# Kernel optimization log

Hardware: AMD Instinct MI355X
Metric: run time of the kernel (lower is better)

## Reference

```python
import jax, jax.numpy as jnp
import numpy as np

INV_COEFF = 25.0
VAR_COEFF = 25.0
COV_COEFF = 1.0


def _cdist(a, b):
    # Euclidean pairwise distance, (B,N,C)x(B,M,C)->(B,N,M)
    a2 = jnp.sum(a * a, axis=-1)[:, :, None]
    b2 = jnp.sum(b * b, axis=-1)[:, None, :]
    d2 = a2 + b2 - 2.0 * jnp.einsum('bnc,bmc->bnm', a, b)
    return jnp.sqrt(jnp.maximum(d2, 0.0))


def _nn_match(input_maps, candidate_maps, distances, num_matches):
    # top-1 NN per input row, then keep the num_matches rows with the
    # smallest NN-distance, preserving original row order (matches the
    # torch sort/sort/mask + masked_select logic exactly).
    min_vals = jnp.min(distances, axis=-1)       # (B, N)
    nn_idx = jnp.argmin(distances, axis=-1)      # (B, N)
    order = jnp.argsort(min_vals, axis=1)[:, :num_matches]   # rows with smallest min-dist
    indices_selected = jnp.sort(order, axis=1)               # restore original order (B, M)
    nn_selected = jnp.take_along_axis(nn_idx, indices_selected, axis=1)  # (B, M)
    filt_in = jnp.take_along_axis(input_maps, indices_selected[..., None], axis=1)
    filt_cand = jnp.take_along_axis(candidate_maps, nn_selected[..., None], axis=1)
    return filt_in, filt_cand


def _vicreg_loss(x, y):
    # x, y: (B, M, C)
    B = x.shape[0]
    C = x.shape[-1]
    repr_loss = INV_COEFF * jnp.mean((x - y) ** 2)
    # gather_center: subtract batch mean (single-device equivalent)
    xc = x - jnp.mean(x, axis=0, keepdims=True)
    yc = y - jnp.mean(y, axis=0, keepdims=True)
    std_x = jnp.sqrt(jnp.var(xc, axis=0, ddof=1) + 1e-4)
    std_y = jnp.sqrt(jnp.var(yc, axis=0, ddof=1) + 1e-4)
    std_loss = VAR_COEFF * (jnp.mean(jax.nn.relu(1.0 - std_x)) / 2
                            + jnp.mean(jax.nn.relu(1.0 - std_y)) / 2)
    # covariance per location: permute to (M, B, C), center over batch
    xp = jnp.transpose(xc, (1, 0, 2))
    yp = jnp.transpose(yc, (1, 0, 2))
    xp = xp - jnp.mean(xp, axis=-2, keepdims=True)
    yp = yp - jnp.mean(yp, axis=-2, keepdims=True)
    cov_x = jnp.einsum('mnc,mnd->mcd', xp, xp) / (B - 1)
    cov_y = jnp.einsum('mnc,mnd->mcd', yp, yp) / (B - 1)
    off = 1.0 - jnp.eye(C, dtype=x.dtype)
    cov_loss = (jnp.sum((cov_x * off) ** 2, axis=(-2, -1)) / C / 2
                + jnp.sum((cov_y * off) ** 2, axis=(-2, -1)) / C / 2)
    cov_loss = COV_COEFF * jnp.mean(cov_loss)
    return repr_loss, std_loss, cov_loss


def _local_loss(maps_1, maps_2, location_1, location_2, num_matches):
    # L2-feature-space NN matching, both directions
    m1f_l2, m1nn_l2 = _nn_match(maps_1, maps_2, _cdist(maps_1, maps_2), num_matches)
    m2f_l2, m2nn_l2 = _nn_match(maps_2, maps_1, _cdist(maps_2, maps_1), num_matches)
    # location-space NN matching, both directions
    loc1 = location_1.reshape(location_1.shape[0], -1, location_1.shape[-1])
    loc2 = location_2.reshape(location_2.shape[0], -1, location_2.shape[-1])
    m1f_loc, m1nn_loc = _nn_match(maps_1, maps_2, _cdist(loc1, loc2), num_matches)
    m2f_loc, m2nn_loc = _nn_match(maps_2, maps_1, _cdist(loc2, loc1), num_matches)
    inv = var = cov = 0.0
    for a, b in ((m1f_l2, m1nn_l2), (m2f_l2, m2nn_l2),
                 (m1f_loc, m1nn_loc), (m2f_loc, m2nn_loc)):
        i, v, c = _vicreg_loss(a, b)
        inv = inv + i
        var = var + v
        cov = cov + c
    return inv + var + cov


def setup_inputs() -> dict:
    key = jax.random.key(0)
    k1, k2, k3, k4 = jax.random.split(key, 4)
    B, HW, C, H = 64, 784, 512, 28
    return {
        'maps_1': jax.random.normal(k1, (B, HW, C), dtype=jnp.float32),
        'maps_2': jax.random.normal(k2, (B, HW, C), dtype=jnp.float32),
        'location_1': jax.random.uniform(k3, (B, H, H, 2), dtype=jnp.float32),
        'location_2': jax.random.uniform(k4, (B, H, H, 2), dtype=jnp.float32),
        'num_matches': 256,
    }


def reference(maps_1, maps_2, location_1, location_2, num_matches):
    return _local_loss(maps_1, maps_2, location_1, location_2, num_matches)
```

## Files before the change

### kernel.cpp

```cpp
#include <hip/hip_runtime.h>
#include <stdint.h>

#define B 64
#define N 784
#define C 512
#define M 256

typedef unsigned long long u64;
typedef unsigned short u16;
typedef __attribute__((ext_vector_type(8))) short short8;
typedef __attribute__((ext_vector_type(4))) float f32x4;

static __device__ __forceinline__ u64 umin64(u64 a, u64 b) { return a < b ? a : b; }

static __device__ __forceinline__ u16 f2bf(float x) {
    unsigned u = __float_as_uint(x);
    return (u16)((u + 0x7FFFu + ((u >> 16) & 1u)) >> 16);
}
static __device__ __forceinline__ float b2f(u16 v) {
    return __uint_as_float((unsigned)v << 16);
}

static __device__ __forceinline__ void gload_lds16(const u16* g, u16* l) {
    __builtin_amdgcn_global_load_lds((const __attribute__((address_space(1))) void*)g,
                                     (__attribute__((address_space(3))) void*)l, 16, 0, 0);
}

__global__ __launch_bounds__(256) void convnorm_kernel(
    const float* __restrict__ m1, const float* __restrict__ m2,
    u16* __restrict__ abf, u16* __restrict__ bbf, float* __restrict__ nrm) {
    int w = blockIdx.x * 4 + (threadIdx.x >> 6);
    int lane = threadIdx.x & 63;
    if (w >= 2 * B * N) return;
    const float* src = (w < B * N) ? m1 : m2;
    u16* dst = (w < B * N) ? abf : bbf;
    int row = (w < B * N) ? w : w - B * N;
    const float4* p = (const float4*)(src + (size_t)row * C);
    u64* q = (u64*)(dst + (size_t)row * C);
    float s = 0.f;
#pragma unroll
    for (int i = 0; i < 2; ++i) {
        int idx = lane + i * 64;
        float4 v = p[idx];
        s += v.x * v.x + v.y * v.y + v.z * v.z + v.w * v.w;
        q[idx] = (u64)f2bf(v.x) | ((u64)f2bf(v.y) << 16) |
                 ((u64)f2bf(v.z) << 32) | ((u64)f2bf(v.w) << 48);
    }
#pragma unroll
    for (int off = 32; off > 0; off >>= 1) s += __shfl_down(s, off, 64);
    if (lane == 0) nrm[w] = s;
}

__global__ __launch_bounds__(256, 2) void feat_mfma_kernel(
    const u16* __restrict__ abf, const u16* __restrict__ bbf,
    const float* __restrict__ nrm, u64* __restrict__ rowkey) {
    int id = blockIdx.x;
    int xcd = id & 7;
    int q = id >> 3;
    int hi = q / 49, t49 = q - hi * 49;
    int b = hi * 8 + xcd;
    int tn = t49 / 7, tm = t49 - tn * 7;

    const int t = threadIdx.x;
    const int lane = t & 63, wv = t >> 6;
    const int wr = wv >> 1, wc = wv & 1;

    __shared__ __align__(16) u16 SM[2][2][128 * 64];
    __shared__ float sNa[128], sNb[128];

    const int row0 = tn * 128, col0 = tm * 128;
    if (t < 128) {
        int n = row0 + t;
        sNa[t] = (n < N) ? nrm[b * N + n] : __builtin_inff();
    } else {
        int m = col0 + (t - 128);
        sNb[t - 128] = (m < N) ? nrm[B * N + b * N + m] : __builtin_inff();
    }

    size_t aofs[4], bofs[4];
    int ldso[4];
#pragma unroll
    for (int s = 0; s < 4; ++s) {
        int c = (wv * 4 + s) * 64 + lane;
        int rl = c >> 3;
        int grp = (c & 7) ^ (rl & 7);
        int ga = row0 + rl; if (ga > N - 1) ga = N - 1;
        int gb = col0 + rl; if (gb > N - 1) gb = N - 1;
        aofs[s] = ((size_t)b * N + ga) * C + grp * 8;
        bofs[s] = ((size_t)b * N + gb) * C + grp * 8;
        ldso[s] = (wv * 4 + s) * 512;
    }

    f32x4 acc[4][4];
#pragma unroll
    for (int i = 0; i < 4; ++i)
#pragma unroll
        for (int j = 0; j < 4; ++j) acc[i][j] = (f32x4){0.f, 0.f, 0.f, 0.f};

#pragma unroll
    for (int s = 0; s < 4; ++s) {
        gload_lds16(abf + aofs[s], &SM[0][0][ldso[s]]);
        gload_lds16(bbf + bofs[s], &SM[0][1][ldso[s]]);
    }
    __syncthreads();

    for (int kt = 0; kt < 8; ++kt) {
        const int cur = kt & 1;
        if (kt < 7) {
            int ke = (kt + 1) * 64;
#pragma unroll
            for (int s = 0; s < 4; ++s) {
                gload_lds16(abf + aofs[s] + ke, &SM[cur ^ 1][0][ldso[s]]);
                gload_lds16(bbf + bofs[s] + ke, &SM[cur ^ 1][1][ldso[s]]);
            }
        }
        const u16* Als = SM[cur][0];
        const u16* Bls = SM[cur][1];
#pragma unroll
        for (int ks = 0; ks < 2; ++ks) {
            short8 afr[4], bfr[4];
            int cb = ks * 4 + (lane >> 4);
#pragma unroll
            for (int f = 0; f < 4; ++f) {
                int ra = wr * 64 + f * 16 + (lane & 15);
                afr[f] = *(const short8*)&Als[ra * 64 + ((cb ^ (ra & 7)) << 3)];
                int rb = wc * 64 + f * 16 + (lane & 15);
                bfr[f] = *(const short8*)&Bls[rb * 64 + ((cb ^ (rb & 7)) << 3)];
            }
#pragma unroll
            for (int fi = 0; fi < 4; ++fi)
#pragma unroll
                for (int fj = 0; fj < 4; ++fj)
                    acc[fi][fj] = __builtin_amdgcn_mfma_f32_16x16x32_bf16(
                        afr[fi], bfr[fj], acc[fi][fj], 0, 0, 0);
        }
        __syncthreads();
    }

    const int g4 = (lane >> 4) << 2;
    float na4[4][4], nb4[4];
#pragma unroll
    for (int fi = 0; fi < 4; ++fi) {
        float4 v = *(const float4*)&sNa[wr * 64 + fi * 16 + g4];
        na4[fi][0] = v.x; na4[fi][1] = v.y; na4[fi][2] = v.z; na4[fi][3] = v.w;
    }
#pragma unroll
    for (int fj = 0; fj < 4; ++fj) nb4[fj] = sNb[wc * 64 + fj * 16 + (lane & 15)];

    u64(*red)[33] = (u64(*)[33])SM;
    u64 ck[4] = {~0ull, ~0ull, ~0ull, ~0ull};
#pragma unroll
    for (int fi = 0; fi < 4; ++fi) {
        int rl = wr * 64 + fi * 16 + g4;
        u64 rk[4] = {~0ull, ~0ull, ~0ull, ~0ull};
#pragma unroll
        for (int fj = 0; fj < 4; ++fj) {
            unsigned colidx = (unsigned)(col0 + wc * 64 + fj * 16 + (lane & 15));
#pragma unroll
            for (int reg = 0; reg < 4; ++reg) {
                float d2 = fmaxf(na4[fi][reg] + nb4[fj] - 2.f * acc[fi][fj][reg], 0.f);
                u64 hv = ((u64)__float_as_uint(d2) << 32);
                rk[reg] = umin64(rk[reg], hv | colidx);
                ck[fj] = umin64(ck[fj], hv | (unsigned)(row0 + rl + reg));
            }
        }
#pragma unroll
        for (int reg = 0; reg < 4; ++reg)
            red[rl + reg][(wc << 4) | (lane & 15)] = rk[reg];
    }
#pragma unroll
    for (int fj = 0; fj < 4; ++fj) {
        u64 best = ck[fj];
        best = umin64(best, __shfl_xor(best, 16, 64));
        best = umin64(best, __shfl_xor(best, 32, 64));
        if (lane < 16) {
            int m = col0 + wc * 64 + fj * 16 + lane;
            if (m < N) atomicMin(&rowkey[(size_t)B * N + (size_t)b * N + m], best);
        }
    }
    __syncthreads();
    if (t < 128) {
        u64 best = red[t][0];
#pragma unroll
        for (int x = 1; x < 32; ++x) best = umin64(best, red[t][x]);
        int n = row0 + t;
        if (n < N) atomicMin(&rowkey[(size_t)b * N + n], best);
    }
}

__global__ __launch_bounds__(256) void loc_dist_kernel(
    const float* __restrict__ l1, const float* __restrict__ l2,
    u64* __restrict__ rowkey) {
    const int dir = blockIdx.z;
    const int b = blockIdx.y;
    const int t = threadIdx.x;
    const int n = blockIdx.x * 256 + t;
    __shared__ float2 s[N];
    const float* Ap = dir ? l2 : l1;
    const float* Bp = dir ? l1 : l2;
    for (int i = t; i < N; i += 256) s[i] = ((const float2*)Bp)[b * N + i];
    __syncthreads();
    if (n >= N) return;
    float2 a = ((const float2*)Ap)[b * N + n];
    float a2 = a.x * a.x + a.y * a.y;
    u64 best = ~0ull;
    for (int mm = 0; mm < N; ++mm) {
        float2 bb = s[mm];
        float d2 = a2 + (bb.x * bb.x + bb.y * bb.y) - 2.f * (a.x * bb.x + a.y * bb.y);
        unsigned vb = __float_as_uint(fmaxf(d2, 0.f));
        u64 kv = ((u64)vb << 32) | (unsigned)mm;
        best = kv < best ? kv : best;
    }
    rowkey[(size_t)(2 + dir) * B * N + (size_t)b * N + n] = best;
}

__global__ __launch_bounds__(256) void select_kernel(
    const u64* __restrict__ rowkey, int* __restrict__ sel_idx,
    int* __restrict__ nn_idx) {
    const int b = blockIdx.x;
    const int dir = blockIdx.y;
    const int t = threadIdx.x;
    __shared__ u64 sk[1024];
    const u64* rk = rowkey + (size_t)dir * B * N + (size_t)b * N;
    for (int i = t; i < 1024; i += 256)
        sk[i] = (i < N) ? ((rk[i] & 0xFFFFFFFF00000000ull) | (unsigned)i) : ~0ull;
    __syncthreads();
    for (unsigned k = 2; k <= 1024; k <<= 1) {
        for (unsigned j = k >> 1; j > 0; j >>= 1) {
            for (unsigned i = t; i < 1024; i += 256) {
                unsigned ixj = i ^ j;
                if (ixj > i) {
                    u64 x = sk[i], y = sk[ixj];
                    bool up = ((i & k) == 0);
                    if ((x > y) == up) { sk[i] = y; sk[ixj] = x; }
                }
            }
            __syncthreads();
        }
    }
    unsigned myidx = (unsigned)(sk[t] & 0xFFFFFFFFull);
    __syncthreads();
    unsigned* si = (unsigned*)sk;
    si[t] = myidx;
    __syncthreads();
    for (unsigned k = 2; k <= 256; k <<= 1) {
        for (unsigned j = k >> 1; j > 0; j >>= 1) {
            unsigned i = t, ixj = i ^ j;
            if (ixj > i) {
                unsigned x = si[i], y = si[ixj];
                bool up = ((i & k) == 0);
                if ((x > y) == up) { si[i] = y; si[ixj] = x; }
            }
            __syncthreads();
        }
    }
    int sel = (int)si[t];
    sel_idx[((size_t)dir * B + b) * M + t] = sel;
    nn_idx[((size_t)dir * B + b) * M + t] = (int)(unsigned)(rk[sel] & 0xFFFFFFFFull);
}

__global__ __launch_bounds__(256) void vicreg_mfma_kernel(
    const u16* __restrict__ abf, const u16* __restrict__ bbf,
    const int* __restrict__ sel_idx, const int* __restrict__ nn_idx,
    float* __restrict__ acc) {
    const int mloc = blockIdx.x;
    const int p = blockIdx.y;
    const int t = threadIdx.x;
    const int l = t & 63, w = t >> 6;

    __shared__ u16 Xs[64 * 128];
    __shared__ u16 Ys[64 * 128];
    __shared__ float colpart[4][128];
    __shared__ float Rsx[64], Rsy[64];
    __shared__ int xi[64], yi[64];
    __shared__ float redsc[4][4];

    if (t < 64) xi[t] = sel_idx[((size_t)p * B + t) * M + mloc];
    else if (t < 128) yi[t - 64] = nn_idx[((size_t)p * B + (t - 64)) * M + mloc];
    if (t < 128) { colpart[0][t] = 0.f; colpart[1][t] = 0.f;
                   colpart[2][t] = 0.f; colpart[3][t] = 0.f; }
    __syncthreads();

    const u16* Xg = (p & 1) ? bbf : abf;
    const u16* Yg = (p & 1) ? abf : bbf;
    unsigned xofs[4], yofs[4];
#pragma unroll
    for (int s = 0; s < 4; ++s) {
        int r = w * 16 + s * 4 + (l >> 4);
        int cs = (l & 15) ^ (r & 15);
        xofs[s] = (unsigned)((r * N + xi[r]) * C + cs * 8);
        yofs[s] = (unsigned)((r * N + yi[r]) * C + cs * 8);
    }

    f32x4 Gx[4], Gy[4], Z;
#pragma unroll
    for (int j = 0; j < 4; ++j) { Gx[j] = (f32x4){0,0,0,0}; Gy[j] = (f32x4){0,0,0,0}; }
    Z = (f32x4){0, 0, 0, 0};
    float stdacc = 0.f, covdacc = 0.f, reprp = 0.f;

    for (int kc = 0; kc < 4; ++kc) {
#pragma unroll
        for (int s = 0; s < 4; ++s) {
            gload_lds16(Xg + xofs[s] + kc * 128, &Xs[(w * 16 + s * 4) * 128]);
            gload_lds16(Yg + yofs[s] + kc * 128, &Ys[(w * 16 + s * 4) * 128]);
        }
        __syncthreads();

#pragma unroll
        for (int ks = 0; ks < 4; ++ks) {
            int cb = ks * 4 + (l >> 4);
            int pe = (cb ^ (l & 15)) << 3;
            short8 ax = *(const short8*)&Xs[((w << 4) + (l & 15)) * 128 + pe];
            short8 ay = *(const short8*)&Ys[((w << 4) + (l & 15)) * 128 + pe];
            short8 bx[4], by[4];
#pragma unroll
            for (int j = 0; j < 4; ++j) {
                bx[j] = *(const short8*)&Xs[(j * 16 + (l & 15)) * 128 + pe];
                by[j] = *(const short8*)&Ys[(j * 16 + (l & 15)) * 128 + pe];
            }
#pragma unroll
            for (int j = 0; j < 4; ++j) {
                Gx[j] = __builtin_amdgcn_mfma_f32_16x16x32_bf16(ax, bx[j], Gx[j], 0, 0, 0);
                Gy[j] = __builtin_amdgcn_mfma_f32_16x16x32_bf16(ay, by[j], Gy[j], 0, 0, 0);
            }
            Z = __builtin_amdgcn_mfma_f32_16x16x32_bf16(ax, ay, Z, 0, 0, 0);
        }

        {
            int cg = l & 31;
            int g2 = (w << 1) + (l >> 5);
            int c4 = cg << 2;
            int cc = c4 >> 3, h = (c4 >> 2) & 1;
            float s1x0 = 0, s1x1 = 0, s1x2 = 0, s1x3 = 0;
            float s2x0 = 0, s2x1 = 0, s2x2 = 0, s2x3 = 0;
            float s1y0 = 0, s1y1 = 0, s1y2 = 0, s1y3 = 0;
            float s2y0 = 0, s2y1 = 0, s2y2 = 0, s2y3 = 0;
#pragma unroll
            for (int rr = 0; rr < 8; ++rr) {
                int r = g2 * 8 + rr;
                int off = r * 128 + ((cc ^ (r & 15)) << 3) + h * 4;
                ushort4 vx = *(const ushort4*)&Xs[off];
                ushort4 vy = *(const ushort4*)&Ys[off];
                float x0 = b2f(vx.x), x1 = b2f(vx.y), x2 = b2f(vx.z), x3 = b2f(vx.w);
                float y0 = b2f(vy.x), y1 = b2f(vy.y), y2 = b2f(vy.z), y3 = b2f(vy.w);
                s1x0 += x0; s1x1 += x1; s1x2 += x2; s1x3 += x3;
                s2x0 = fmaf(x0, x0, s2x0); s2x1 = fmaf(x1, x1, s2x1);
                s2x2 = fmaf(x2, x2, s2x2); s2x3 = fmaf(x3, x3, s2x3);
                s1y0 += y0; s1y1 += y1; s1y2 += y2; s1y3 += y3;
                s2y0 = fmaf(y0, y0, s2y0); s2y1 = fmaf(y1, y1, s2y1);
                s2y2 = fmaf(y2, y2, s2y2); s2y3 = fmaf(y3, y3, s2y3);
            }
            s1x0 += __shfl_xor(s1x0, 32, 64); s1x1 += __shfl_xor(s1x1, 32, 64);
            s1x2 += __shfl_xor(s1x2, 32, 64); s1x3 += __shfl_xor(s1x3, 32, 64);
            s2x0 += __shfl_xor(s2x0, 32, 64); s2x1 += __shfl_xor(s2x1, 32, 64);
            s2x2 += __shfl_xor(s2x2, 32, 64); s2x3 += __shfl_xor(s2x3, 32, 64);
            s1y0 += __shfl_xor(s1y0, 32, 64); s1y1 += __shfl_xor(s1y1, 32, 64);
            s1y2 += __shfl_xor(s1y2, 32, 64); s1y3 += __shfl_xor(s1y3, 32, 64);
            s2y0 += __shfl_xor(s2y0, 32, 64); s2y1 += __shfl_xor(s2y1, 32, 64);
            s2y2 += __shfl_xor(s2y2, 32, 64); s2y3 += __shfl_xor(s2y3, 32, 64);
            if (l < 32) {
                atomicAdd(&colpart[0][c4 + 0], s1x0); atomicAdd(&colpart[0][c4 + 1], s1x1);
                atomicAdd(&colpart[0][c4 + 2], s1x2); atomicAdd(&colpart[0][c4 + 3], s1x3);
                atomicAdd(&colpart[1][c4 + 0], s2x0); atomicAdd(&colpart[1][c4 + 1], s2x1);
                atomicAdd(&colpart[1][c4 + 2], s2x2); atomicAdd(&colpart[1][c4 + 3], s2x3);
                atomicAdd(&colpart[2][c4 + 0], s1y0); atomicAdd(&colpart[2][c4 + 1], s1y1);
                atomicAdd(&colpart[2][c4 + 2], s1y2); atomicAdd(&colpart[2][c4 + 3], s1y3);
                atomicAdd(&colpart[3][c4 + 0], s2y0); atomicAdd(&colpart[3][c4 + 1], s2y1);
                atomicAdd(&colpart[3][c4 + 2], s2y2); atomicAdd(&colpart[3][c4 + 3], s2y3);
            }
        }
        __syncthreads();

        if (t < 128) {
            float s1x = colpart[0][t], s2x = colpart[1][t];
            float s1y = colpart[2][t], s2y = colpart[3][t];
            float sx = s2x - s1x * s1x * (1.f / 64.f);
            float sy = s2y - s1y * s1y * (1.f / 64.f);
            stdacc += fmaxf(0.f, 1.f - sqrtf(sx * (1.f / 63.f) + 1e-4f)) +
                      fmaxf(0.f, 1.f - sqrtf(sy * (1.f / 63.f) + 1e-4f));
            covdacc += sx * sx + sy * sy;
            reprp += s2x + s2y;
            colpart[0][t] = 0.f; colpart[1][t] = 0.f;
            colpart[2][t] = 0.f; colpart[3][t] = 0.f;
        }
    }

    float zd = 0.f;
    {
        int rbase = (l >> 4) << 2, col = l & 15;
#pragma unroll
        for (int reg = 0; reg < 4; ++reg)
            zd += (col == rbase + reg) ? Z[reg] : 0.f;
    }
    float rsx[4], rsy[4];
#pragma unroll
    for (int reg = 0; reg < 4; ++reg) {
        rsx[reg] = Gx[0][reg] + Gx[1][reg] + Gx[2][reg] + Gx[3][reg];
        rsy[reg] = Gy[0][reg] + Gy[1][reg] + Gy[2][reg] + Gy[3][reg];
    }
#pragma unroll
    for (int off = 1; off < 16; off <<= 1)
#pragma unroll
        for (int reg = 0; reg < 4; ++reg) {
            rsx[reg] += __shfl_xor(rsx[reg], off, 64);
            rsy[reg] += __shfl_xor(rsy[reg], off, 64);
        }
    if ((l & 15) == 0) {
#pragma unroll
        for (int reg = 0; reg < 4; ++reg) {
            Rsx[(w << 4) + ((l >> 4) << 2) + reg] = rsx[reg];
            Rsy[(w << 4) + ((l >> 4) << 2) + reg] = rsy[reg];
        }
    }
    __syncthreads();
    float Tx = 0.f, Ty = 0.f;
    for (int i = 0; i < 64; ++i) { Tx += Rsx[i]; Ty += Rsy[i]; }
    float tX = Tx * (1.f / 4096.f), tY = Ty * (1.f / 4096.f);
    float kn = 0.f;
#pragma unroll
    for (int j = 0; j < 4; ++j) {
        float cX = Rsx[(j << 4) + (l & 15)] * (1.f / 64.f);
        float cY = Rsy[(j << 4) + (l & 15)] * (1.f / 64.f);
#pragma unroll
        for (int reg = 0; reg < 4; ++reg) {
            float K1 = Gx[j][reg] - rsx[reg] * (1.f / 64.f) - cX + tX;
            kn = fmaf(K1, K1, kn);
            float K2 = Gy[j][reg] - rsy[reg] * (1.f / 64.f) - cY + tY;
            kn = fmaf(K2, K2, kn);
        }
    }

    float v0 = reprp - 2.f * zd, v1 = stdacc, v2 = covdacc, v3 = kn;
#pragma unroll
    for (int off = 1; off < 64; off <<= 1) {
        v0 += __shfl_xor(v0, off, 64);
        v1 += __shfl_xor(v1, off, 64);
        v2 += __shfl_xor(v2, off, 64);
        v3 += __shfl_xor(v3, off, 64);
    }
    if (l == 0) { redsc[w][0] = v0; redsc[w][1] = v1; redsc[w][2] = v2; redsc[w][3] = v3; }
    __syncthreads();
    if (t == 0) {
        float r0 = 0, r1 = 0, r2 = 0, r3 = 0;
#pragma unroll
        for (int ww = 0; ww < 4; ++ww) {
            r0 += redsc[ww][0]; r1 += redsc[ww][1];
            r2 += redsc[ww][2]; r3 += redsc[ww][3];
        }
        atomicAdd(&acc[0], r0);
        atomicAdd(&acc[1], r1);
        atomicAdd(&acc[2], r3 - r2);
    }
}

__global__ __launch_bounds__(256) void norms_kernel(const float* __restrict__ m1,
                                                    const float* __restrict__ m2,
                                                    float* __restrict__ nrm) {
    int w = blockIdx.x * 4 + (threadIdx.x >> 6);
    int lane = threadIdx.x & 63;
    if (w >= 2 * B * N) return;
    const float* src = (w < B * N) ? m1 : m2;
    int row = (w < B * N) ? w : w - B * N;
    const float4* p = (const float4*)(src + (size_t)row * C);
    float s = 0.f;
#pragma unroll
    for (int i = 0; i < 2; ++i) {
        float4 v = p[lane + i * 64];
        s += v.x * v.x + v.y * v.y + v.z * v.z + v.w * v.w;
    }
#pragma unroll
    for (int off = 32; off > 0; off >>= 1) s += __shfl_down(s, off, 64);
    if (lane == 0) nrm[w] = s;
}

__global__ __launch_bounds__(256) void feat_dist_kernel(
    const float* __restrict__ m1, const float* __restrict__ m2,
    const float* __restrict__ nrm, u64* __restrict__ rowkey) {
    const int b = blockIdx.z;
    const int tn = blockIdx.x, tm = blockIdx.y;
    __shared__ float As[64][68];
    __shared__ float Bt[64][68];
    __shared__ u64 red[64][16];
    const int t = threadIdx.x;
    const int ty = t >> 4, tx = t & 15;
    float acc[4][4] = {};
    const float* A = m1 + (size_t)b * N * C;
    const float* Bm = m2 + (size_t)b * N * C;

    for (int k0 = 0; k0 < C; k0 += 64) {
#pragma unroll
        for (int it = 0; it < 4; ++it) {
            int idx = t + it * 256;
            int r = idx >> 4, cc = (idx & 15) << 2;
            int n = tn * 64 + r;
            float4 v = make_float4(0.f, 0.f, 0.f, 0.f);
            if (n < N) v = *(const float4*)(A + (size_t)n * C + k0 + cc);
            *(float4*)&As[r][cc] = v;
            int mm = tm * 64 + r;
            float4 w = make_float4(0.f, 0.f, 0.f, 0.f);
            if (mm < N) w = *(const float4*)(Bm + (size_t)mm * C + k0 + cc);
            Bt[cc + 0][r] = w.x; Bt[cc + 1][r] = w.y;
            Bt[cc + 2][r] = w.z; Bt[cc + 3][r] = w.w;
        }
        __syncthreads();
#pragma unroll 4
        for (int kq = 0; kq < 64; kq += 4) {
            float aa[4][4], bb[4][4];
#pragma unroll
            for (int i = 0; i < 4; ++i) {
                float4 v = *(const float4*)&As[ty * 4 + i][kq];
                aa[i][0] = v.x; aa[i][1] = v.y; aa[i][2] = v.z; aa[i][3] = v.w;
            }
#pragma unroll
            for (int qq = 0; qq < 4; ++qq) {
                float4 v = *(const float4*)&Bt[kq + qq][tx * 4];
                bb[qq][0] = v.x; bb[qq][1] = v.y; bb[qq][2] = v.z; bb[qq][3] = v.w;
            }
#pragma unroll
            for (int qq = 0; qq < 4; ++qq)
#pragma unroll
                for (int i = 0; i < 4; ++i)
#pragma unroll
                    for (int j = 0; j < 4; ++j)
                        acc[i][j] = fmaf(aa[i][qq], bb[qq][j], acc[i][j]);
        }
        __syncthreads();
    }

    u64 rk[4] = {~0ull, ~0ull, ~0ull, ~0ull};
    u64 ck[4] = {~0ull, ~0ull, ~0ull, ~0ull};
    const float* nr1 = nrm;
    const float* nr2 = nrm + B * N;
#pragma unroll
    for (int i = 0; i < 4; ++i) {
        int n = tn * 64 + ty * 4 + i;
        if (n >= N) continue;
        float a2 = nr1[b * N + n];
#pragma unroll
        for (int j = 0; j < 4; ++j) {
            int mm = tm * 64 + tx * 4 + j;
            if (mm >= N) continue;
            float b2 = nr2[b * N + mm];
            float d2 = a2 + b2 - 2.f * acc[i][j];
            unsigned vb = __float_as_uint(fmaxf(d2, 0.f));
            u64 kv = ((u64)vb << 32);
            rk[i] = umin64(rk[i], kv | (unsigned)mm);
            ck[j] = umin64(ck[j], kv | (unsigned)n);
        }
    }
#pragma unroll
    for (int i = 0; i < 4; ++i) red[ty * 4 + i][tx] = rk[i];
    __syncthreads();
    if (t < 64) {
        u64 best = red[t][0];
#pragma unroll
        for (int x = 1; x < 16; ++x) best = umin64(best, red[t][x]);
        int n = tn * 64 + t;
        if (n < N && best != ~0ull)
            atomicMin(&rowkey[(size_t)b * N + n], best);
    }
    __syncthreads();
#pragma unroll
    for (int j = 0; j < 4; ++j) red[tx * 4 + j][ty] = ck[j];
    __syncthreads();
    if (t < 64) {
        u64 best = red[t][0];
#pragma unroll
        for (int x = 1; x < 16; ++x) best = umin64(best, red[t][x]);
        int mm = tm * 64 + t;
        if (mm < N && best != ~0ull)
            atomicMin(&rowkey[(size_t)B * N + (size_t)b * N + mm], best);
    }
}

__device__ __forceinline__ float blockReduce(float v, float* redb, int t) {
    __syncthreads();
    redb[t] = v;
    __syncthreads();
    for (int s = 128; s > 0; s >>= 1) {
        if (t < s) redb[t] += redb[t + s];
        __syncthreads();
    }
    return redb[0];
}

__global__ __launch_bounds__(256) void vicreg_kernel(
    const float* __restrict__ m1, const float* __restrict__ m2,
    const int* __restrict__ sel_idx, const int* __restrict__ nn_idx,
    float* __restrict__ acc) {
    const int mloc = blockIdx.x;
    const int p = blockIdx.y;
    const int t = threadIdx.x;
    const float* X = (p & 1) ? m2 : m1;
    const float* Y = (p & 1) ? m1 : m2;
    __shared__ float Xs[64][65];
    __shared__ float Ys[64][65];
    __shared__ int xi[64], yi[64];
    __shared__ float pst[192][5];
    __shared__ float Rs[64];
    __shared__ float Tsh;
    __shared__ float redb[256];

    if (t < 64) {
        xi[t] = sel_idx[((size_t)p * B + t) * M + mloc];
        yi[t] = nn_idx[((size_t)p * B + t) * M + mloc];
    }
    __syncthreads();

    float Gx[4][4] = {}, Gy[4][4] = {};
    float stdx = 0, stdy = 0, covdx = 0, covdy = 0, repr = 0;
    const int i0 = (t >> 4) << 2, j0 = (t & 15) << 2;

    for (int c0 = 0; c0 < C; c0 += 64) {
#pragma unroll
        for (int it = 0; it < 4; ++it) {
            int fidx = t + it * 256;
            int r = fidx >> 4, cc = (fidx & 15) << 2;
            float4 v = *(const float4*)(X + ((size_t)r * N + xi[r]) * C + c0 + cc);
            Xs[r][cc] = v.x; Xs[r][cc + 1] = v.y; Xs[r][cc + 2] = v.z; Xs[r][cc + 3] = v.w;
            float4 w = *(const float4*)(Y + ((size_t)r * N + yi[r]) * C + c0 + cc);
            Ys[r][cc] = w.x; Ys[r][cc + 1] = w.y; Ys[r][cc + 2] = w.z; Ys[r][cc + 3] = w.w;
        }
        __syncthreads();
#pragma unroll 4
        for (int k = 0; k < 64; ++k) {
            float ax[4], bx[4], ay[4], by[4];
#pragma unroll
            for (int i = 0; i < 4; ++i) { ax[i] = Xs[i0 + i][k]; ay[i] = Ys[i0 + i][k]; }
#pragma unroll
            for (int j = 0; j < 4; ++j) { bx[j] = Xs[j0 + j][k]; by[j] = Ys[j0 + j][k]; }
#pragma unroll
            for (int i = 0; i < 4; ++i)
#pragma unroll
                for (int j = 0; j < 4; ++j) {
                    Gx[i][j] = fmaf(ax[i], bx[j], Gx[i][j]);
                    Gy[i][j] = fmaf(ay[i], by[j], Gy[i][j]);
                }
        }
        {
            float s1x = 0, s2x = 0, s1y = 0, s2y = 0, sxy = 0;
            int col = t & 63, g = t >> 6;
            for (int r = g * 16; r < g * 16 + 16; ++r) {
                float xv = Xs[r][col], yv = Ys[r][col];
                s1x += xv; s2x += xv * xv;
                s1y += yv; s2y += yv * yv;
                sxy += xv * yv;
            }
            if (g) {
                float* qq = pst[(g - 1) * 64 + col];
                qq[0] = s1x; qq[1] = s2x; qq[2] = s1y; qq[3] = s2y; qq[4] = sxy;
            }
            __syncthreads();
            if (g == 0) {
#pragma unroll
                for (int gg = 0; gg < 3; ++gg) {
                    float* qq = pst[gg * 64 + col];
                    s1x += qq[0]; s2x += qq[1]; s1y += qq[2]; s2y += qq[3]; sxy += qq[4];
                }
                float xb = s1x * (1.f / 64.f);
                float sx = s2x - 64.f * xb * xb;
                float yb = s1y * (1.f / 64.f);
                float sy = s2y - 64.f * yb * yb;
                stdx += fmaxf(0.f, 1.f - sqrtf(sx * (1.f / 63.f) + 1e-4f));
                stdy += fmaxf(0.f, 1.f - sqrtf(sy * (1.f / 63.f) + 1e-4f));
                covdx += sx * sx;
                covdy += sy * sy;
                repr += s2x + s2y - 2.f * sxy;
            }
            __syncthreads();
        }
    }

    float knx = 0.f, kny = 0.f;
    float (*Gs)[65] = (float(*)[65]) & Xs[0][0];
    __syncthreads();
#pragma unroll
    for (int i = 0; i < 4; ++i)
#pragma unroll
        for (int j = 0; j < 4; ++j) Gs[i0 + i][j0 + j] = Gx[i][j];
    __syncthreads();
    if (t < 64) {
        float r = 0;
        for (int j = 0; j < 64; ++j) r += Gs[t][j];
        Rs[t] = r;
    }
    __syncthreads();
    if (t < 64) {
        float r = Rs[t];
#pragma unroll
        for (int off = 32; off > 0; off >>= 1) r += __shfl_down(r, off, 64);
        if (t == 0) Tsh = r;
    }
    __syncthreads();
    {
        float T = Tsh * (1.f / 4096.f);
#pragma unroll
        for (int i = 0; i < 4; ++i)
#pragma unroll
            for (int j = 0; j < 4; ++j) {
                float Kij = Gx[i][j] - (Rs[i0 + i] + Rs[j0 + j]) * (1.f / 64.f) + T;
                knx = fmaf(Kij, Kij, knx);
            }
    }
    __syncthreads();
#pragma unroll
    for (int i = 0; i < 4; ++i)
#pragma unroll
        for (int j = 0; j < 4; ++j) Gs[i0 + i][j0 + j] = Gy[i][j];
    __syncthreads();
    if (t < 64) {
        float r = 0;
        for (int j = 0; j < 64; ++j) r += Gs[t][j];
        Rs[t] = r;
    }
    __syncthreads();
    if (t < 64) {
        float r = Rs[t];
#pragma unroll
        for (int off = 32; off > 0; off >>= 1) r += __shfl_down(r, off, 64);
        if (t == 0) Tsh = r;
    }
    __syncthreads();
    {
        float T = Tsh * (1.f / 4096.f);
#pragma unroll
        for (int i = 0; i < 4; ++i)
#pragma unroll
            for (int j = 0; j < 4; ++j) {
                float Kij = Gy[i][j] - (Rs[i0 + i] + Rs[j0 + j]) * (1.f / 64.f) + T;
                kny = fmaf(Kij, Kij, kny);
            }
    }

    float v_repr = blockReduce(repr, redb, t);
    float v_std = blockReduce(stdx + stdy, redb, t);
    float v_covd = blockReduce(covdx + covdy, redb, t);
    float v_kn = blockReduce(knx + kny, redb, t);
    if (t == 0) {
        atomicAdd(&acc[0], v_repr);
        atomicAdd(&acc[1], v_std);
        atomicAdd(&acc[2], v_kn - v_covd);
    }
}

__global__ void finalize_kernel(const float* __restrict__ acc, float* __restrict__ out) {
    if (threadIdx.x == 0 && blockIdx.x == 0) {
        float repr = 25.f * acc[0] / ((float)B * (float)M * (float)C);
        float stdl = 12.5f * acc[1] / ((float)M * (float)C);
        float cov = acc[2] / (63.f * 63.f * (float)C * 2.f) / (float)M;
        out[0] = repr + stdl + cov;
    }
}

extern "C" void kernel_launch(void* const* d_in, const int* in_sizes, int n_in,
                              void* d_out, int out_size, void* d_ws, size_t ws_size,
                              hipStream_t stream) {
    const float* m1 = (const float*)d_in[0];
    const float* m2 = (const float*)d_in[1];
    const float* l1 = (const float*)d_in[2];
    const float* l2 = (const float*)d_in[3];
    float* out = (float*)d_out;
    char* ws = (char*)d_ws;

    u64* rowkey = (u64*)ws;
    size_t off = (size_t)4 * B * N * sizeof(u64);
    float* nrm = (float*)(ws + off); off += (size_t)2 * B * N * sizeof(float);
    int* sel_idx = (int*)(ws + off); off += (size_t)4 * B * M * sizeof(int);
    int* nn_idx = (int*)(ws + off);  off += (size_t)4 * B * M * sizeof(int);
    float* acc = (float*)(ws + off); off += 256;
    off = (off + 255) & ~(size_t)255;
    u16* abf = (u16*)(ws + off);
    u16* bbf = abf + (size_t)B * N * C;
    size_t need = off + (size_t)2 * B * N * C * sizeof(u16);
    bool use_mfma = ws_size >= need;

    hipMemsetAsync(rowkey, 0xFF, (size_t)4 * B * N * sizeof(u64), stream);
    hipMemsetAsync(acc, 0, 32, stream);
    if (use_mfma) {
        convnorm_kernel<<<dim3(2 * B * N / 4), dim3(256), 0, stream>>>(m1, m2, abf, bbf, nrm);
        feat_mfma_kernel<<<dim3(64 * 49), dim3(256), 0, stream>>>(abf, bbf, nrm, rowkey);
    } else {
        norms_kernel<<<dim3(2 * B * N / 4), dim3(256), 0, stream>>>(m1, m2, nrm);
        feat_dist_kernel<<<dim3(13, 13, B), dim3(256), 0, stream>>>(m1, m2, nrm, rowkey);
    }
    loc_dist_kernel<<<dim3((N + 255) / 256, B, 2), dim3(256), 0, stream>>>(l1, l2, rowkey);
    select_kernel<<<dim3(B, 4), dim3(256), 0, stream>>>(rowkey, sel_idx, nn_idx);
    if (use_mfma) {
        vicreg_mfma_kernel<<<dim3(M, 4), dim3(256), 0, stream>>>(abf, bbf, sel_idx, nn_idx, acc);
    } else {
        vicreg_kernel<<<dim3(M, 4), dim3(256), 0, stream>>>(m1, m2, sel_idx, nn_idx, acc);
    }
    finalize_kernel<<<dim3(1), dim3(64), 0, stream>>>(acc, out);
}
```

Measured before the change: 303.2 us.

## Double-buffer LDS loads in vicreg kernel, drop shared atomics, precompute norms

The vicreg MFMA kernel now double-buffers the X/Y LDS tiles, so the next K-chunk's global-to-LDS loads are issued while the current chunk is computed. Per-column sums are written into per-wave slots and summed afterwards, replacing shared-memory atomics. The 64-element total is reduced with wave shuffles instead of a serial loop. The location distance kernel precomputes each point's squared norm into LDS and uses fused multiply-adds; launch bounds and extra syncs are added, and LDS use grows.

```diff
diff --git a/kernel.cpp b/kernel.cpp
--- a/kernel.cpp
+++ b/kernel.cpp
@@ -195,20 +195,24 @@
     const int b = blockIdx.y;
     const int t = threadIdx.x;
     const int n = blockIdx.x * 256 + t;
-    __shared__ float2 s[N];
+    __shared__ __align__(16) float4 s4[N];
     const float* Ap = dir ? l2 : l1;
     const float* Bp = dir ? l1 : l2;
-    for (int i = t; i < N; i += 256) s[i] = ((const float2*)Bp)[b * N + i];
+    for (int i = t; i < N; i += 256) {
+        float2 qv = ((const float2*)Bp)[b * N + i];
+        s4[i] = make_float4(qv.x, qv.y, qv.x * qv.x + qv.y * qv.y, 0.f);
+    }
     __syncthreads();
     if (n >= N) return;
     float2 a = ((const float2*)Ap)[b * N + n];
     float a2 = a.x * a.x + a.y * a.y;
+    float nax = -2.f * a.x, nay = -2.f * a.y;
     u64 best = ~0ull;
+#pragma unroll 4
     for (int mm = 0; mm < N; ++mm) {
-        float2 bb = s[mm];
-        float d2 = a2 + (bb.x * bb.x + bb.y * bb.y) - 2.f * (a.x * bb.x + a.y * bb.y);
-        unsigned vb = __float_as_uint(fmaxf(d2, 0.f));
-        u64 kv = ((u64)vb << 32) | (unsigned)mm;
+        float4 v = s4[mm];
+        float d2 = fmaxf(fmaf(nax, v.x, fmaf(nay, v.y, a2 + v.z)), 0.f);
+        u64 kv = ((u64)__float_as_uint(d2) << 32) | (unsigned)mm;
         best = kv < best ? kv : best;
     }
     rowkey[(size_t)(2 + dir) * B * N + (size_t)b * N + n] = best;
@@ -259,7 +263,7 @@
     nn_idx[((size_t)dir * B + b) * M + t] = (int)(unsigned)(rk[sel] & 0xFFFFFFFFull);
 }
 
-__global__ __launch_bounds__(256) void vicreg_mfma_kernel(
+__global__ __launch_bounds__(256, 2) void vicreg_mfma_kernel(
     const u16* __restrict__ abf, const u16* __restrict__ bbf,
     const int* __restrict__ sel_idx, const int* __restrict__ nn_idx,
     float* __restrict__ acc) {
@@ -268,28 +272,28 @@
     const int t = threadIdx.x;
     const int l = t & 63, w = t >> 6;
 
-    __shared__ u16 Xs[64 * 128];
-    __shared__ u16 Ys[64 * 128];
-    __shared__ float colpart[4][128];
+    __shared__ __align__(16) u16 Xs[2][64 * 128];
+    __shared__ __align__(16) u16 Ys[2][64 * 128];
+    __shared__ float colpart[4][4][128];
     __shared__ float Rsx[64], Rsy[64];
     __shared__ int xi[64], yi[64];
     __shared__ float redsc[4][4];
 
     if (t < 64) xi[t] = sel_idx[((size_t)p * B + t) * M + mloc];
     else if (t < 128) yi[t - 64] = nn_idx[((size_t)p * B + (t - 64)) * M + mloc];
-    if (t < 128) { colpart[0][t] = 0.f; colpart[1][t] = 0.f;
-                   colpart[2][t] = 0.f; colpart[3][t] = 0.f; }
     __syncthreads();
 
     const u16* Xg = (p & 1) ? bbf : abf;
     const u16* Yg = (p & 1) ? abf : bbf;
     unsigned xofs[4], yofs[4];
+    int ldst[4];
 #pragma unroll
     for (int s = 0; s < 4; ++s) {
         int r = w * 16 + s * 4 + (l >> 4);
         int cs = (l & 15) ^ (r & 15);
         xofs[s] = (unsigned)((r * N + xi[r]) * C + cs * 8);
         yofs[s] = (unsigned)((r * N + yi[r]) * C + cs * 8);
+        ldst[s] = (w * 16 + s * 4) * 128;
     }
 
     f32x4 Gx[4], Gy[4], Z;
@@ -298,25 +302,37 @@
     Z = (f32x4){0, 0, 0, 0};
     float stdacc = 0.f, covdacc = 0.f, reprp = 0.f;
 
+#pragma unroll
+    for (int s = 0; s < 4; ++s) {
+        gload_lds16(Xg + xofs[s], &Xs[0][ldst[s]]);
+        gload_lds16(Yg + yofs[s], &Ys[0][ldst[s]]);
+    }
+    __syncthreads();
+
     for (int kc = 0; kc < 4; ++kc) {
-#pragma unroll
-        for (int s = 0; s < 4; ++s) {
-            gload_lds16(Xg + xofs[s] + kc * 128, &Xs[(w * 16 + s * 4) * 128]);
-            gload_lds16(Yg + yofs[s] + kc * 128, &Ys[(w * 16 + s * 4) * 128]);
-        }
-        __syncthreads();
+        const int cur = kc & 1;
+        if (kc < 3) {
+            int ke = (kc + 1) * 128;
+#pragma unroll
+            for (int s = 0; s < 4; ++s) {
+                gload_lds16(Xg + xofs[s] + ke, &Xs[cur ^ 1][ldst[s]]);
+                gload_lds16(Yg + yofs[s] + ke, &Ys[cur ^ 1][ldst[s]]);
+            }
+        }
+        const u16* Xc = Xs[cur];
+        const u16* Yc = Ys[cur];
 
 #pragma unroll
         for (int ks = 0; ks < 4; ++ks) {
             int cb = ks * 4 + (l >> 4);
             int pe = (cb ^ (l & 15)) << 3;
-            short8 ax = *(const short8*)&Xs[((w << 4) + (l & 15)) * 128 + pe];
-            short8 ay = *(const short8*)&Ys[((w << 4) + (l & 15)) * 128 + pe];
+            short8 ax = *(const short8*)&Xc[((w << 4) + (l & 15)) * 128 + pe];
+            short8 ay = *(const short8*)&Yc[((w << 4) + (l & 15)) * 128 + pe];
             short8 bx[4], by[4];
 #pragma unroll
             for (int j = 0; j < 4; ++j) {
-                bx[j] = *(const short8*)&Xs[(j * 16 + (l & 15)) * 128 + pe];
-                by[j] = *(const short8*)&Ys[(j * 16 + (l & 15)) * 128 + pe];
+                bx[j] = *(const short8*)&Xc[(j * 16 + (l & 15)) * 128 + pe];
+                by[j] = *(const short8*)&Yc[(j * 16 + (l & 15)) * 128 + pe];
             }
 #pragma unroll
             for (int j = 0; j < 4; ++j) {
@@ -327,10 +343,9 @@
         }
 
         {
-            int cg = l & 31;
+            int c4 = (l & 31) << 2;
+            int cc = c4 >> 3, h = (c4 >> 2) & 1;
             int g2 = (w << 1) + (l >> 5);
-            int c4 = cg << 2;
-            int cc = c4 >> 3, h = (c4 >> 2) & 1;
             float s1x0 = 0, s1x1 = 0, s1x2 = 0, s1x3 = 0;
             float s2x0 = 0, s2x1 = 0, s2x2 = 0, s2x3 = 0;
             float s1y0 = 0, s1y1 = 0, s1y2 = 0, s1y3 = 0;
@@ -339,8 +354,8 @@
             for (int rr = 0; rr < 8; ++rr) {
                 int r = g2 * 8 + rr;
                 int off = r * 128 + ((cc ^ (r & 15)) << 3) + h * 4;
-                ushort4 vx = *(const ushort4*)&Xs[off];
-                ushort4 vy = *(const ushort4*)&Ys[off];
+                ushort4 vx = *(const ushort4*)&Xc[off];
+                ushort4 vy = *(const ushort4*)&Yc[off];
                 float x0 = b2f(vx.x), x1 = b2f(vx.y), x2 = b2f(vx.z), x3 = b2f(vx.w);
                 float y0 = b2f(vy.x), y1 = b2f(vy.y), y2 = b2f(vy.z), y3 = b2f(vy.w);
                 s1x0 += x0; s1x1 += x1; s1x2 += x2; s1x3 += x3;
@@ -359,30 +374,29 @@
             s2y0 += __shfl_xor(s2y0, 32, 64); s2y1 += __shfl_xor(s2y1, 32, 64);
             s2y2 += __shfl_xor(s2y2, 32, 64); s2y3 += __shfl_xor(s2y3, 32, 64);
             if (l < 32) {
-                atomicAdd(&colpart[0][c4 + 0], s1x0); atomicAdd(&colpart[0][c4 + 1], s1x1);
-                atomicAdd(&colpart[0][c4 + 2], s1x2); atomicAdd(&colpart[0][c4 + 3], s1x3);
-                atomicAdd(&colpart[1][c4 + 0], s2x0); atomicAdd(&colpart[1][c4 + 1], s2x1);
-                atomicAdd(&colpart[1][c4 + 2], s2x2); atomicAdd(&colpart[1][c4 + 3], s2x3);
-                atomicAdd(&colpart[2][c4 + 0], s1y0); atomicAdd(&colpart[2][c4 + 1], s1y1);
-                atomicAdd(&colpart[2][c4 + 2], s1y2); atomicAdd(&colpart[2][c4 + 3], s1y3);
-                atomicAdd(&colpart[3][c4 + 0], s2y0); atomicAdd(&colpart[3][c4 + 1], s2y1);
-                atomicAdd(&colpart[3][c4 + 2], s2y2); atomicAdd(&colpart[3][c4 + 3], s2y3);
+                *(float4*)&colpart[w][0][c4] = make_float4(s1x0, s1x1, s1x2, s1x3);
+                *(float4*)&colpart[w][1][c4] = make_float4(s2x0, s2x1, s2x2, s2x3);
+                *(float4*)&colpart[w][2][c4] = make_float4(s1y0, s1y1, s1y2, s1y3);
+                *(float4*)&colpart[w][3][c4] = make_float4(s2y0, s2y1, s2y2, s2y3);
             }
         }
         __syncthreads();
 
         if (t < 128) {
-            float s1x = colpart[0][t], s2x = colpart[1][t];
-            float s1y = colpart[2][t], s2y = colpart[3][t];
+            float s1x = 0, s2x = 0, s1y = 0, s2y = 0;
+#pragma unroll
+            for (int ww = 0; ww < 4; ++ww) {
+                s1x += colpart[ww][0][t]; s2x += colpart[ww][1][t];
+                s1y += colpart[ww][2][t]; s2y += colpart[ww][3][t];
+            }
             float sx = s2x - s1x * s1x * (1.f / 64.f);
             float sy = s2y - s1y * s1y * (1.f / 64.f);
             stdacc += fmaxf(0.f, 1.f - sqrtf(sx * (1.f / 63.f) + 1e-4f)) +
                       fmaxf(0.f, 1.f - sqrtf(sy * (1.f / 63.f) + 1e-4f));
             covdacc += sx * sx + sy * sy;
             reprp += s2x + s2y;
-            colpart[0][t] = 0.f; colpart[1][t] = 0.f;
-            colpart[2][t] = 0.f; colpart[3][t] = 0.f;
-        }
+        }
+        __syncthreads();
     }
 
     float zd = 0.f;
@@ -413,9 +427,13 @@
         }
     }
     __syncthreads();
-    float Tx = 0.f, Ty = 0.f;
-    for (int i = 0; i < 64; ++i) { Tx += Rsx[i]; Ty += Rsy[i]; }
-    float tX = Tx * (1.f / 4096.f), tY = Ty * (1.f / 4096.f);
+    float myx = Rsx[l], myy = Rsy[l];
+#pragma unroll
+    for (int off = 1; off < 64; off <<= 1) {
+        myx += __shfl_xor(myx, off, 64);
+        myy += __shfl_xor(myy, off, 64);
+    }
+    float tX = myx * (1.f / 4096.f), tY = myy * (1.f / 4096.f);
     float kn = 0.f;
 #pragma unroll
     for (int j = 0; j < 4; ++j) {
```

After: 264.8 us. -12.7%, faster.
